# Optimization experiments

Hardware: AMD Instinct MI355X
Metric: run time of the kernel (lower is better)

## Reference

```python
import math
import jax, jax.numpy as jnp
import numpy as np

N_FEATURES = 32
DEGREE = 3
BATCH = 8192
N_POLY = math.comb(N_FEATURES + DEGREE, DEGREE)  # 6545


def _build_monomial_indices(n_features, degree):
    """Static (numpy) indices replicating the Pascal-triangle recursion in TaylorMap._poly.

    For degree level i (i = 1..degree-1), the original code appends, for each feature f,
    x[:, f] * prev_block[:, :comb(i+f, i)].  We flatten that into gather index arrays so the
    whole block is one vectorized gather+multiply instead of a Python loop of slices/concats.
    """
    levels = []
    for i in range(1, degree):
        counts = np.array([math.comb(i + f, i) for f in range(n_features)], dtype=np.int64)
        f_idx = np.repeat(np.arange(n_features, dtype=np.int64), counts)
        m_idx = np.concatenate([np.arange(c, dtype=np.int64) for c in counts])
        levels.append((f_idx, m_idx))
    return levels

_LEVELS = _build_monomial_indices(N_FEATURES, DEGREE)


def _poly(x):
    # x: [B, n].  Returns [B, n_poly] monomial features in the exact order of TaylorMap._poly.
    b = x.shape[0]
    parts = [jnp.ones((b, 1), x.dtype), x]
    prev = x
    for f_idx, m_idx in _LEVELS:  # static loop over degree levels (degree-1 iterations)
        new = x[:, f_idx] * prev[:, m_idx]  # [B, comb(n+i, i+1)-ish block]
        parts.append(new)
        prev = new
    return jnp.concatenate(parts, axis=-1)


def setup_inputs() -> dict:
    key = jax.random.key(0)
    kx, kw = jax.random.split(key)
    x = jax.random.normal(kx, (BATCH, N_FEATURES), dtype=jnp.float32)
    # learned weight W: [n_poly, n_features] (default init is zeros; use small randn for a
    # non-degenerate numerical baseline)
    W = jax.random.normal(kw, (N_POLY, N_FEATURES), dtype=jnp.float32) * 0.02
    return {"x": x, "W": W}


def reference(x, W):
    # TaylorMap(x) = x * residual + poly(x) @ W   (residual=True)
    return x + _poly(x) @ W
```

## Files before the change

kernel.cpp:

```cpp
#include <hip/hip_runtime.h>
#include <cstdint>
#include <cstddef>
#include <utility>


#define NF 32
#define NPOLY 6545
#define NSTEPS 448
#define NREAL 417
#define NOCT 834
#define NDESC 1024
#define CHUNK 56
#define TSTRIDE 576
#define D2OFF 40
#define XDSTRIDE 34

#define XD_OFF    36864
#define SMEM_BYTES 39040

typedef _Float16 f16x8 __attribute__((ext_vector_type(8)));
typedef float f32x16 __attribute__((ext_vector_type(16)));
typedef short short8v __attribute__((ext_vector_type(8)));

#define D2N 528
struct D2I { uint8_t a[D2N]; uint8_t b[D2N]; };
constexpr D2I build_d2i() {
    D2I t{};
    int k = 0;
    for (int f = 0; f < NF; ++f)
        for (int m = 0; m <= f; ++m) { t.a[k] = (uint8_t)f; t.b[k] = (uint8_t)m; ++k; }
    return t;
}
constexpr D2I D2T = build_d2i();

struct Desc { uint32_t d[NDESC]; };
constexpr Desc build_desc() {
    Desc D{};
    int u = 0;
    for (int o = 0; o < 72; ++o)
        D.d[u++] = (uint32_t)(o * 16);
    for (int f = 0; f < NF; ++f) {
        int cnt = (f + 1) * (f + 2) / 2;
        for (int j8 = 0; j8 < (cnt + 7) / 8; ++j8)
            D.d[u++] = (uint32_t)((D2OFF + 8 * j8) * 2) | ((uint32_t)((1 + f) * 2) << 16);
    }
    while (u < NDESC) D.d[u++] = 0u;
    return D;
}
__device__ const Desc DESC_G = build_desc();

struct Oldk { int16_t v[NSTEPS * 16]; };
constexpr Oldk build_oldk() {
    Oldk K{};
    int k = 0;
    for (int ti = 0; ti < 576; ++ti) {
        int old;
        if (ti == 0) old = 0;
        else if (ti <= 32) old = ti;
        else if (ti >= D2OFF && ti < D2OFF + D2N) old = 33 + (ti - D2OFF);
        else old = -1;
        K.v[k++] = (int16_t)old;
    }
    for (int f = 0; f < NF; ++f) {
        int cnt = (f + 1) * (f + 2) / 2;
        int off3 = 0;
        for (int g = 0; g < f; ++g) off3 += (g + 1) * (g + 2) / 2;
        int oc = (cnt + 7) / 8;
        for (int m = 0; m < oc * 8; ++m)
            K.v[k++] = (int16_t)(m < cnt ? 561 + off3 + m : -1);
    }
    while (k < NSTEPS * 16) K.v[k++] = (int16_t)-1;
    return K;
}
__device__ const Oldk OLDK_G = build_oldk();

template<int TI>
__device__ __forceinline__ _Float16 tval(const float (&xr)[NF]) {
    if constexpr (TI == 0) return (_Float16)1.0f;
    else if constexpr (TI >= 1 && TI <= 32) return (_Float16)xr[TI - 1];
    else if constexpr (TI >= D2OFF && TI < D2OFF + D2N) {
        constexpr int m = TI - D2OFF;
        return (_Float16)(xr[D2T.a[m]] * xr[D2T.b[m]]);
    } else return (_Float16)0.0f;
}

template<int O, int... Js>
__device__ __forceinline__ void put_oct(std::integer_sequence<int, Js...>,
                                        const float (&xr)[NF], _Float16* trow, int r) {
    f16x8 v = { tval<O * 8 + Js>(xr)... };
    int slot = (O & ~7) | ((O ^ r) & 7);
    *(f16x8*)(trow + slot * 8) = v;
}

template<int BASE, int... Os>
__device__ __forceinline__ void p1_octs(std::integer_sequence<int, Os...>,
                                        const float (&xr)[NF], _Float16* trow, int r) {
    (put_oct<BASE + Os>(std::make_integer_sequence<int, 8>{}, xr, trow, r), ...);
}

template<int V>
__device__ __forceinline__ void xdw(const float (&xr)[NF], _Float16* xdrow) {
    if constexpr (V == 0) xdrow[0] = (_Float16)1.0f;
    else if constexpr (V <= 32) xdrow[V] = (_Float16)xr[V - 1];
}

template<int G>
__device__ __forceinline__ void p1_group(const float (&xr)[NF], _Float16* trow,
                                         _Float16* xdrow, int r) {
    if constexpr (G < 8)
        p1_octs<G * 5>(std::make_integer_sequence<int, 5>{}, xr, trow, r);
    else
        p1_octs<40 + (G - 8) * 4>(std::make_integer_sequence<int, 4>{}, xr, trow, r);
    xdw<2 * G>(xr, xdrow);
    xdw<2 * G + 1>(xr, xdrow);
    if constexpr (G == 15) xdw<32>(xr, xdrow);
}

__global__ void prep(const float* __restrict__ W, _Float16* __restrict__ Wh) {
    int id = blockIdx.x * 256 + threadIdx.x;
    int step = id >> 6, rem = id & 63, hs = rem >> 5, n = rem & 31;
    int k0 = step * 16 + hs * 8;
    short8v olds = *(const short8v*)(OLDK_G.v + k0);
    f16x8 v;
#pragma unroll
    for (int j = 0; j < 8; ++j) {
        int old = olds[j];
        v[j] = (_Float16)(old >= 0 ? W[old * 32 + n] : 0.0f);
    }
    *(f16x8*)(Wh + (size_t)id * 8) = v;
}

__global__ __launch_bounds__(512, 2) void gemm(const float* __restrict__ x,
                                               const _Float16* __restrict__ Wh,
                                               float* __restrict__ out) {
    __shared__ __align__(16) unsigned char smem[SMEM_BYTES];
    _Float16* t  = (_Float16*)smem;
    _Float16* xd = (_Float16*)(smem + XD_OFF);

    const int tid = threadIdx.x;
    const int wave = __builtin_amdgcn_readfirstlane(tid >> 6);
    const int lane = tid & 63;
    const int hsel = lane >> 5, r = lane & 31;
    const int mtile = blockIdx.x;

    {
        const int pr = tid & 31, g = tid >> 5;
        float xr[NF];
        const float4* xp = (const float4*)(x + (size_t)(mtile * 32 + pr) * NF);
#pragma unroll
        for (int i = 0; i < 8; ++i) {
            float4 v = xp[i];
            xr[4 * i + 0] = v.x; xr[4 * i + 1] = v.y;
            xr[4 * i + 2] = v.z; xr[4 * i + 3] = v.w;
        }
        _Float16* trow = t + pr * TSTRIDE;
        _Float16* xdrow = xd + pr * XDSTRIDE;
        switch (g) {
            case  0: p1_group< 0>(xr, trow, xdrow, pr); break;
            case  1: p1_group< 1>(xr, trow, xdrow, pr); break;
            case  2: p1_group< 2>(xr, trow, xdrow, pr); break;
            case  3: p1_group< 3>(xr, trow, xdrow, pr); break;
            case  4: p1_group< 4>(xr, trow, xdrow, pr); break;
            case  5: p1_group< 5>(xr, trow, xdrow, pr); break;
            case  6: p1_group< 6>(xr, trow, xdrow, pr); break;
            case  7: p1_group< 7>(xr, trow, xdrow, pr); break;
            case  8: p1_group< 8>(xr, trow, xdrow, pr); break;
            case  9: p1_group< 9>(xr, trow, xdrow, pr); break;
            case 10: p1_group<10>(xr, trow, xdrow, pr); break;
            case 11: p1_group<11>(xr, trow, xdrow, pr); break;
            case 12: p1_group<12>(xr, trow, xdrow, pr); break;
            case 13: p1_group<13>(xr, trow, xdrow, pr); break;
            case 14: p1_group<14>(xr, trow, xdrow, pr); break;
            default: p1_group<15>(xr, trow, xdrow, pr); break;
        }
    }

    const int s0 = __builtin_amdgcn_readfirstlane(wave * CHUNK);
    uint32_t vD0 = DESC_G.d[2 * (s0 + lane)];
    uint32_t vD1 = DESC_G.d[2 * (s0 + lane) + 1];

    __syncthreads();

    const char* trowB = (const char*)t + r * (TSTRIDE * 2);
    const char* xdrowB = (const char*)xd + r * (XDSTRIDE * 2);
    const char* wpB = (const char*)Wh + lane * 16;
    const uint32_t rx = (uint32_t)((r & 7) << 4);

    f32x16 acc0, acc1;
#pragma unroll
    for (int i = 0; i < 16; ++i) { acc0[i] = 0.0f; acc1[i] = 0.0f; }

#define DSEL(IDX) (hsel ? __builtin_amdgcn_readlane(vD1, (IDX)) \
                        : __builtin_amdgcn_readlane(vD0, (IDX)))

    f16x8 araw0, araw1, araw2, araw3, araw4, araw5, araw6, araw7;
    f16x8 breg0, breg1, breg2, breg3, breg4, breg5, breg6, breg7;
    _Float16 xs0, xs1, xs2, xs3, xs4, xs5, xs6, xs7;

#define LOADSLOT(P, IDX) do {                                                 \
    uint32_t d_ = DSEL(IDX);                                                  \
    araw##P = *(const f16x8*)(trowB + ((d_ & 0xffffu) ^ rx));                 \
    xs##P   = *(const _Float16*)(xdrowB + (d_ >> 16));                        \
    breg##P = *(const f16x8*)(wpB + (size_t)(s0 + (IDX)) * 1024);             \
} while (0)

    LOADSLOT(0, 0); LOADSLOT(1, 1); LOADSLOT(2, 2); LOADSLOT(3, 3);
    LOADSLOT(4, 4); LOADSLOT(5, 5); LOADSLOT(6, 6); LOADSLOT(7, 7);

#define BODY(P, IDX, A) do {                                                  \
    f16x8 xsv_ = { xs##P, xs##P, xs##P, xs##P, xs##P, xs##P, xs##P, xs##P };  \
    f16x8 a_ = araw##P * xsv_;                                                \
    f16x8 bu_ = breg##P;                                                      \
    LOADSLOT(P, (IDX) + 8);   \
    A = __builtin_amdgcn_mfma_f32_32x32x16_f16(a_, bu_, A, 0, 0, 0);          \
} while (0)

#pragma unroll
    for (int i = 0; i < 7; ++i) {
        BODY(0, 8 * i + 0, acc0);
        BODY(1, 8 * i + 1, acc1);
        BODY(2, 8 * i + 2, acc0);
        BODY(3, 8 * i + 3, acc1);
        BODY(4, 8 * i + 4, acc0);
        BODY(5, 8 * i + 5, acc1);
        BODY(6, 8 * i + 6, acc0);
        BODY(7, 8 * i + 7, acc1);
    }
#undef BODY
#undef LOADSLOT
#undef DSEL

#pragma unroll
    for (int i = 0; i < 16; ++i) acc0[i] += acc1[i];

    __syncthreads();
    float* red = (float*)smem;
    float* bank = red + wave * 1024;
#pragma unroll
    for (int reg = 0; reg < 16; ++reg) {
        int rr = (reg & 3) + 8 * (reg >> 2) + 4 * hsel;
        bank[rr * 32 + r] = acc0[reg];
    }
    __syncthreads();
    const float* xt = x + (size_t)mtile * 1024;
    float* op = out + (size_t)mtile * 1024;
#pragma unroll
    for (int i = 0; i < 2; ++i) {
        int e = tid + i * 512;
        float v = red[e] + red[1024 + e] + red[2048 + e] + red[3072 + e]
                + red[4096 + e] + red[5120 + e] + red[6144 + e] + red[7168 + e]
                + xt[e];
        op[e] = v;
    }
}

extern "C" void kernel_launch(void* const* d_in, const int* in_sizes, int n_in,
                              void* d_out, int out_size, void* d_ws, size_t ws_size,
                              hipStream_t stream) {
    (void)in_sizes; (void)n_in; (void)out_size; (void)ws_size;
    const float* x = (const float*)d_in[0];
    const float* W = (const float*)d_in[1];
    float* out = (float*)d_out;
    _Float16* Wh = (_Float16*)d_ws;

    prep<<<112, 256, 0, stream>>>(W, Wh);
    gemm<<<256, 512, 0, stream>>>(x, Wh, out);
}
```

Measured before the change: 67.67 us.

## Fuse weight conversion into GEMM by reading fp32 W directly with descriptors

```diff
diff --git a/kernel.cpp b/kernel.cpp
--- a/kernel.cpp
+++ b/kernel.cpp
@@ -7,7 +7,6 @@
 #define NF 32
 #define NPOLY 6545
 #define NSTEPS 448
-#define NREAL 417
 #define NOCT 834
 #define NDESC 1024
 #define CHUNK 56
@@ -20,7 +19,6 @@
 
 typedef _Float16 f16x8 __attribute__((ext_vector_type(8)));
 typedef float f32x16 __attribute__((ext_vector_type(16)));
-typedef short short8v __attribute__((ext_vector_type(8)));
 
 #define D2N 528
 struct D2I { uint8_t a[D2N]; uint8_t b[D2N]; };
@@ -33,46 +31,50 @@
 }
 constexpr D2I D2T = build_d2i();
 
-struct Desc { uint32_t d[NDESC]; };
-constexpr Desc build_desc() {
-    Desc D{};
-    int u = 0;
-    for (int o = 0; o < 72; ++o)
-        D.d[u++] = (uint32_t)(o * 16);
+struct Desc2 { uint32_t t[NDESC]; uint32_t w[NDESC]; };
+constexpr Desc2 build_desc2() {
+    Desc2 D{};
+    uint32_t tt[NOCT] = {}; uint32_t ww[NOCT] = {};
+    int n = 0;
+    for (int o = 0; o < 72; ++o) {
+        int old0, cnt;
+        if (o == 0)       { old0 = 0;                cnt = 8; }
+        else if (o <= 3)  { old0 = o * 8;            cnt = 8; }
+        else if (o == 4)  { old0 = 32;               cnt = 1; }
+        else if (o <= 70) { old0 = 33 + (o * 8 - 40); cnt = 8; }
+        else              { old0 = 0;                cnt = 0; }
+        tt[n] = (uint32_t)(o * 16);
+        ww[n] = (uint32_t)(old0 * 128) | ((uint32_t)cnt << 28);
+        ++n;
+    }
     for (int f = 0; f < NF; ++f) {
-        int cnt = (f + 1) * (f + 2) / 2;
-        for (int j8 = 0; j8 < (cnt + 7) / 8; ++j8)
-            D.d[u++] = (uint32_t)((D2OFF + 8 * j8) * 2) | ((uint32_t)((1 + f) * 2) << 16);
-    }
-    while (u < NDESC) D.d[u++] = 0u;
-    return D;
-}
-__device__ const Desc DESC_G = build_desc();
-
-struct Oldk { int16_t v[NSTEPS * 16]; };
-constexpr Oldk build_oldk() {
-    Oldk K{};
-    int k = 0;
-    for (int ti = 0; ti < 576; ++ti) {
-        int old;
-        if (ti == 0) old = 0;
-        else if (ti <= 32) old = ti;
-        else if (ti >= D2OFF && ti < D2OFF + D2N) old = 33 + (ti - D2OFF);
-        else old = -1;
-        K.v[k++] = (int16_t)old;
-    }
-    for (int f = 0; f < NF; ++f) {
-        int cnt = (f + 1) * (f + 2) / 2;
+        int cntf = (f + 1) * (f + 2) / 2;
         int off3 = 0;
         for (int g = 0; g < f; ++g) off3 += (g + 1) * (g + 2) / 2;
-        int oc = (cnt + 7) / 8;
-        for (int m = 0; m < oc * 8; ++m)
-            K.v[k++] = (int16_t)(m < cnt ? 561 + off3 + m : -1);
-    }
-    while (k < NSTEPS * 16) K.v[k++] = (int16_t)-1;
-    return K;
-}
-__device__ const Oldk OLDK_G = build_oldk();
+        for (int j8 = 0; j8 < (cntf + 7) / 8; ++j8) {
+            int rem = cntf - 8 * j8;
+            int cnt = rem >= 8 ? 8 : rem;
+            tt[n] = (uint32_t)((D2OFF + 8 * j8) * 2) | ((uint32_t)((1 + f) * 2) << 16);
+            ww[n] = (uint32_t)((561 + off3 + 8 * j8) * 128) | ((uint32_t)cnt << 28);
+            ++n;
+        }
+    }
+    int u = 0;
+    for (int i = 0; i < n; ++i)
+        if ((ww[i] >> 28) == 8u) { D.t[u] = tt[i]; D.w[u] = ww[i]; ++u; }
+    for (int i = 0; i < n; ++i)
+        if ((ww[i] >> 28) != 8u) { D.t[u] = tt[i]; D.w[u] = ww[i]; ++u; }
+    while (u < NDESC) { D.t[u] = 0u; D.w[u] = 0u; ++u; }
+    return D;
+}
+__device__ const Desc2 DESC2_G = build_desc2();
+
+constexpr int count_fulls() {
+    int F = 70;
+    for (int f = 0; f < NF; ++f) F += ((f + 1) * (f + 2) / 2) / 8;
+    return F;
+}
+static_assert(count_fulls() >= 2 * 7 * CHUNK, "fast waves must see only full descs");
 
 template<int TI>
 __device__ __forceinline__ _Float16 tval(const float (&xr)[NF]) {
@@ -116,23 +118,95 @@
     if constexpr (G == 15) xdw<32>(xr, xdrow);
 }
 
-__global__ void prep(const float* __restrict__ W, _Float16* __restrict__ Wh) {
-    int id = blockIdx.x * 256 + threadIdx.x;
-    int step = id >> 6, rem = id & 63, hs = rem >> 5, n = rem & 31;
-    int k0 = step * 16 + hs * 8;
-    short8v olds = *(const short8v*)(OLDK_G.v + k0);
-    f16x8 v;
-#pragma unroll
-    for (int j = 0; j < 8; ++j) {
-        int old = olds[j];
-        v[j] = (_Float16)(old >= 0 ? W[old * 32 + n] : 0.0f);
-    }
-    *(f16x8*)(Wh + (size_t)id * 8) = v;
-}
-
-__global__ __launch_bounds__(512, 2) void gemm(const float* __restrict__ x,
-                                               const _Float16* __restrict__ Wh,
-                                               float* __restrict__ out) {
+#define DSEL(IDX) (hsel ? __builtin_amdgcn_readlane(vD1, (IDX)) \
+                        : __builtin_amdgcn_readlane(vD0, (IDX)))
+#define WSEL(IDX) (hsel ? __builtin_amdgcn_readlane(vW1, (IDX)) \
+                        : __builtin_amdgcn_readlane(vW0, (IDX)))
+
+#define DECLSLOT(P) f16x8 araw##P; _Float16 xs##P; uint32_t wd##P; \
+    float b##P##0, b##P##1, b##P##2, b##P##3, b##P##4, b##P##5, b##P##6, b##P##7;
+
+#define LOADSLOT(P, IDX) do {                                                 \
+    uint32_t d_ = DSEL(IDX);                                                  \
+    uint32_t w_ = WSEL(IDX);                                                  \
+    araw##P = *(const f16x8*)(trowB + ((d_ & 0xffffu) ^ rx));                 \
+    xs##P   = *(const _Float16*)(xdrowB + (d_ >> 16));                        \
+    wd##P   = w_;                                                             \
+    const char* wp_ = wcolB + (w_ & 0x0fffffffu);                             \
+    b##P##0 = *(const float*)(wp_ +   0);                                     \
+    b##P##1 = *(const float*)(wp_ + 128);                                     \
+    b##P##2 = *(const float*)(wp_ + 256);                                     \
+    b##P##3 = *(const float*)(wp_ + 384);                                     \
+    b##P##4 = *(const float*)(wp_ + 512);                                     \
+    b##P##5 = *(const float*)(wp_ + 640);                                     \
+    b##P##6 = *(const float*)(wp_ + 768);                                     \
+    b##P##7 = *(const float*)(wp_ + 896);                                     \
+} while (0)
+
+#define BODY(P, IDX, A) do {                                                  \
+    f16x8 am_;                                                                \
+    if constexpr (MASKED) {                                                   \
+        uint32_t cnt_ = wd##P >> 28;                                          \
+        _Float16 z_ = (_Float16)0.0f;                                         \
+        f16x8 xm_;                                                            \
+        xm_[0] = (0u < cnt_) ? xs##P : z_;                                    \
+        xm_[1] = (1u < cnt_) ? xs##P : z_;                                    \
+        xm_[2] = (2u < cnt_) ? xs##P : z_;                                    \
+        xm_[3] = (3u < cnt_) ? xs##P : z_;                                    \
+        xm_[4] = (4u < cnt_) ? xs##P : z_;                                    \
+        xm_[5] = (5u < cnt_) ? xs##P : z_;                                    \
+        xm_[6] = (6u < cnt_) ? xs##P : z_;                                    \
+        xm_[7] = (7u < cnt_) ? xs##P : z_;                                    \
+        am_ = araw##P * xm_;                                                  \
+    } else {                                                                  \
+        f16x8 xsv_ = { xs##P, xs##P, xs##P, xs##P, xs##P, xs##P, xs##P, xs##P }; \
+        am_ = araw##P * xsv_;                                                 \
+    }                                                                         \
+    f16x8 bu_;                                                                \
+    bu_[0] = (_Float16)b##P##0;                                               \
+    bu_[1] = (_Float16)b##P##1;                                               \
+    bu_[2] = (_Float16)b##P##2;                                               \
+    bu_[3] = (_Float16)b##P##3;                                               \
+    bu_[4] = (_Float16)b##P##4;                                               \
+    bu_[5] = (_Float16)b##P##5;                                               \
+    bu_[6] = (_Float16)b##P##6;                                               \
+    bu_[7] = (_Float16)b##P##7;                                               \
+    LOADSLOT(P, (IDX) + 8);   \
+    A = __builtin_amdgcn_mfma_f32_32x32x16_f16(am_, bu_, A, 0, 0, 0);         \
+} while (0)
+
+template<bool MASKED>
+__device__ __forceinline__ void run_chunk(uint32_t vD0, uint32_t vD1,
+                                          uint32_t vW0, uint32_t vW1,
+                                          const char* trowB, const char* xdrowB,
+                                          const char* wcolB, uint32_t rx, int hsel,
+                                          f32x16& acc0, f32x16& acc1) {
+    DECLSLOT(0) DECLSLOT(1) DECLSLOT(2) DECLSLOT(3)
+    DECLSLOT(4) DECLSLOT(5) DECLSLOT(6) DECLSLOT(7)
+
+    LOADSLOT(0, 0); LOADSLOT(1, 1); LOADSLOT(2, 2); LOADSLOT(3, 3);
+    LOADSLOT(4, 4); LOADSLOT(5, 5); LOADSLOT(6, 6); LOADSLOT(7, 7);
+
+#pragma unroll
+    for (int i = 0; i < 7; ++i) {
+        BODY(0, 8 * i + 0, acc0);
+        BODY(1, 8 * i + 1, acc1);
+        BODY(2, 8 * i + 2, acc0);
+        BODY(3, 8 * i + 3, acc1);
+        BODY(4, 8 * i + 4, acc0);
+        BODY(5, 8 * i + 5, acc1);
+        BODY(6, 8 * i + 6, acc0);
+        BODY(7, 8 * i + 7, acc1);
+    }
+}
+
+#undef BODY
+#undef LOADSLOT
+#undef DECLSLOT
+
+__global__ __launch_bounds__(512, 2) void fused(const float* __restrict__ x,
+                                                const float* __restrict__ W,
+                                                float* __restrict__ out) {
     __shared__ __align__(16) unsigned char smem[SMEM_BYTES];
     _Float16* t  = (_Float16*)smem;
     _Float16* xd = (_Float16*)(smem + XD_OFF);
@@ -176,59 +250,26 @@
     }
 
     const int s0 = __builtin_amdgcn_readfirstlane(wave * CHUNK);
-    uint32_t vD0 = DESC_G.d[2 * (s0 + lane)];
-    uint32_t vD1 = DESC_G.d[2 * (s0 + lane) + 1];
+    uint32_t vD0 = DESC2_G.t[2 * (s0 + lane)];
+    uint32_t vD1 = DESC2_G.t[2 * (s0 + lane) + 1];
+    uint32_t vW0 = DESC2_G.w[2 * (s0 + lane)];
+    uint32_t vW1 = DESC2_G.w[2 * (s0 + lane) + 1];
 
     __syncthreads();
 
     const char* trowB = (const char*)t + r * (TSTRIDE * 2);
     const char* xdrowB = (const char*)xd + r * (XDSTRIDE * 2);
-    const char* wpB = (const char*)Wh + lane * 16;
+    const char* wcolB = (const char*)W + r * 4;
     const uint32_t rx = (uint32_t)((r & 7) << 4);
 
     f32x16 acc0, acc1;
 #pragma unroll
     for (int i = 0; i < 16; ++i) { acc0[i] = 0.0f; acc1[i] = 0.0f; }
 
-#define DSEL(IDX) (hsel ? __builtin_amdgcn_readlane(vD1, (IDX)) \
-                        : __builtin_amdgcn_readlane(vD0, (IDX)))
-
-    f16x8 araw0, araw1, araw2, araw3, araw4, araw5, araw6, araw7;
-    f16x8 breg0, breg1, breg2, breg3, breg4, breg5, breg6, breg7;
-    _Float16 xs0, xs1, xs2, xs3, xs4, xs5, xs6, xs7;
-
-#define LOADSLOT(P, IDX) do {                                                 \
-    uint32_t d_ = DSEL(IDX);                                                  \
-    araw##P = *(const f16x8*)(trowB + ((d_ & 0xffffu) ^ rx));                 \
-    xs##P   = *(const _Float16*)(xdrowB + (d_ >> 16));                        \
-    breg##P = *(const f16x8*)(wpB + (size_t)(s0 + (IDX)) * 1024);             \
-} while (0)
-
-    LOADSLOT(0, 0); LOADSLOT(1, 1); LOADSLOT(2, 2); LOADSLOT(3, 3);
-    LOADSLOT(4, 4); LOADSLOT(5, 5); LOADSLOT(6, 6); LOADSLOT(7, 7);
-
-#define BODY(P, IDX, A) do {                                                  \
-    f16x8 xsv_ = { xs##P, xs##P, xs##P, xs##P, xs##P, xs##P, xs##P, xs##P };  \
-    f16x8 a_ = araw##P * xsv_;                                                \
-    f16x8 bu_ = breg##P;                                                      \
-    LOADSLOT(P, (IDX) + 8);   \
-    A = __builtin_amdgcn_mfma_f32_32x32x16_f16(a_, bu_, A, 0, 0, 0);          \
-} while (0)
-
-#pragma unroll
-    for (int i = 0; i < 7; ++i) {
-        BODY(0, 8 * i + 0, acc0);
-        BODY(1, 8 * i + 1, acc1);
-        BODY(2, 8 * i + 2, acc0);
-        BODY(3, 8 * i + 3, acc1);
-        BODY(4, 8 * i + 4, acc0);
-        BODY(5, 8 * i + 5, acc1);
-        BODY(6, 8 * i + 6, acc0);
-        BODY(7, 8 * i + 7, acc1);
-    }
-#undef BODY
-#undef LOADSLOT
-#undef DSEL
+    if (wave == 7)
+        run_chunk<true >(vD0, vD1, vW0, vW1, trowB, xdrowB, wcolB, rx, hsel, acc0, acc1);
+    else
+        run_chunk<false>(vD0, vD1, vW0, vW1, trowB, xdrowB, wcolB, rx, hsel, acc0, acc1);
 
 #pragma unroll
     for (int i = 0; i < 16; ++i) acc0[i] += acc1[i];
@@ -257,12 +298,10 @@
 extern "C" void kernel_launch(void* const* d_in, const int* in_sizes, int n_in,
                               void* d_out, int out_size, void* d_ws, size_t ws_size,
                               hipStream_t stream) {
-    (void)in_sizes; (void)n_in; (void)out_size; (void)ws_size;
+    (void)in_sizes; (void)n_in; (void)out_size; (void)d_ws; (void)ws_size;
     const float* x = (const float*)d_in[0];
     const float* W = (const float*)d_in[1];
     float* out = (float*)d_out;
-    _Float16* Wh = (_Float16*)d_ws;
-
-    prep<<<112, 256, 0, stream>>>(W, Wh);
-    gemm<<<256, 512, 0, stream>>>(x, Wh, out);
-}
+
+    fused<<<256, 512, 0, stream>>>(x, W, out);
+}
```

Result: slower. 72.76 us (+7.5%).
